# Performance work log

Hardware: AMD Instinct MI355X
Metric: run time of the kernel (lower is better)

Reference implementation:

```python
import jax, jax.numpy as jnp
import numpy as np

B = 2          # graphs (images)
GRID = 13      # patches per spatial dim -> N = 169 patches per image
N = GRID * GRID
NN = B * N     # total nodes
C = 256        # hidden_dim / out_channels per head
H = 4          # attention heads
L = 3          # GAT layers
LRELU_SLOPE = 0.2
LN_EPS = 1e-5


def _dense_edges():
    # fully-connected directed graph (i != j) per image, as in create_graph
    idx = np.arange(N)
    src, dst = np.meshgrid(idx, idx, indexing='ij')
    mask = src != dst
    src, dst = src[mask], dst[mask]              # [N*(N-1)]
    offs = (np.arange(B) * N)[:, None]
    e_src = (src[None, :] + offs).reshape(-1)
    e_dst = (dst[None, :] + offs).reshape(-1)
    return e_src.astype(np.int32), e_dst.astype(np.int32)


def setup_inputs() -> dict:
    key = jax.random.key(0)
    ks = jax.random.split(key, 8)
    s = 0.05
    e_src, e_dst = _dense_edges()
    return {
        'x':   jax.random.normal(ks[0], (NN, C), jnp.float32),
        'Wl':  jax.random.normal(ks[1], (L, C, H * C), jnp.float32) * s,
        'bl':  jnp.zeros((L, H * C), jnp.float32),
        'Wr':  jax.random.normal(ks[2], (L, C, H * C), jnp.float32) * s,
        'br':  jnp.zeros((L, H * C), jnp.float32),
        'att': jax.random.normal(ks[3], (L, H, C), jnp.float32) * s,
        'bias': jnp.zeros((L, C), jnp.float32),
        'ln_g': jnp.ones((L, C), jnp.float32),
        'ln_b': jnp.zeros((L, C), jnp.float32),
        'W1':  jax.random.normal(ks[4], (L, C, 2 * C), jnp.float32) * s,
        'b1':  jnp.zeros((L, 2 * C), jnp.float32),
        'W2':  jax.random.normal(ks[5], (L, 2 * C, C), jnp.float32) * s,
        'b2':  jnp.zeros((L, C), jnp.float32),
        'edge_src': jnp.asarray(e_src),
        'edge_dst': jnp.asarray(e_dst),
        'batch_ids': jnp.repeat(jnp.arange(B, dtype=jnp.int32), N),
    }


def _gatv2(x, Wl, bl, Wr, br, att, bias, src, dst, n_nodes):
    # PyG GATv2Conv, concat=False (mean over heads)
    xl = (x @ Wl + bl).reshape(n_nodes, H, C)   # source transform
    xr = (x @ Wr + br).reshape(n_nodes, H, C)   # target transform
    e = jax.nn.leaky_relu(xl[src] + xr[dst], LRELU_SLOPE)     # [E,H,C]
    logits = jnp.einsum('ehc,hc->eh', e, att)                 # [E,H]
    m = jax.ops.segment_max(logits, dst, num_segments=n_nodes)
    a = jnp.exp(logits - m[dst])
    z = jax.ops.segment_sum(a, dst, num_segments=n_nodes)
    alpha = a / (z[dst] + 1e-16)                              # softmax per target
    msg = alpha[:, :, None] * xl[src]                         # [E,H,C]
    agg = jax.ops.segment_sum(msg, dst, num_segments=n_nodes) # [N,H,C]
    return agg.mean(axis=1) + bias


def _layernorm(x, g, b):
    mu = x.mean(-1, keepdims=True)
    var = jnp.mean((x - mu) ** 2, -1, keepdims=True)
    return (x - mu) * jax.lax.rsqrt(var + LN_EPS) * g + b


def reference(x, Wl, bl, Wr, br, att, bias, ln_g, ln_b, W1, b1, W2, b2,
              edge_src, edge_dst, batch_ids):
    n_nodes = x.shape[0]
    for l in range(L):
        residual = x
        h = _gatv2(x, Wl[l], bl[l], Wr[l], br[l], att[l], bias[l],
                   edge_src, edge_dst, n_nodes)
        h = _layernorm(h, ln_g[l], ln_b[l])
        mlp = jnp.maximum(h @ W1[l] + b1[l], 0.0) @ W2[l] + b2[l]
        x = residual + mlp
    # global mean pool per graph
    sums = jax.ops.segment_sum(x, batch_ids, num_segments=B)
    cnts = jax.ops.segment_sum(jnp.ones((n_nodes, 1), x.dtype), batch_ids,
                               num_segments=B)
    return sums / cnts
```

## Files before the change

kernel.cpp:

```cpp
#include <hip/hip_runtime.h>
#include <hip/hip_bf16.h>

typedef __hip_bfloat16 bf16;
typedef __attribute__((ext_vector_type(8))) short short8v;
typedef __attribute__((ext_vector_type(4))) float float4v;

#define NNODES 169
#define NNTOT  338
#define CH     256
#define NH     4
#define NL     3
#define SPAD   176
#define LN_EPS 1e-5f

__device__ __forceinline__ float b2f(bf16 v) { return __bfloat162float(v); }
__device__ __forceinline__ float lrelu(float v) { return fmaxf(v, 0.2f * v); }
__device__ __forceinline__ float ldm(const void* p, size_t i, int isbf) {
    return isbf ? b2f(((const bf16*)p)[i]) : ((const float*)p)[i];
}
__device__ __forceinline__ short f2bf(float f) {
    union { float f; unsigned u; } x; x.f = f;
    return (short)((x.u + 0x7FFFu + ((x.u >> 16) & 1u)) >> 16);
}
__device__ __forceinline__ int sniff_bf(const void* lng) {
    return ((((const unsigned*)lng)[0] & 0xFFFFu) == 0x3F80u) ? 1 : 0;
}

__global__ __launch_bounds__(256) void k_wt(
    const void* __restrict__ Wl, const void* __restrict__ Wr,
    const void* __restrict__ W1, const void* __restrict__ W2,
    short* __restrict__ wlT, short* __restrict__ wrT,
    short* __restrict__ w1T, short* __restrict__ w2T,
    const void* __restrict__ lng)
{
    __shared__ float s_t[32][33];
    const int isbf = sniff_bf(lng);
    const int z = blockIdx.z, mat = z & 3, l = z >> 2;
    const void* src; short* dst; int K, N;
    if      (mat == 0) { src = Wl; dst = wlT; K = CH;     N = NH * CH; }
    else if (mat == 1) { src = Wr; dst = wrT; K = CH;     N = NH * CH; }
    else if (mat == 2) { src = W1; dst = w1T; K = CH;     N = 2 * CH;  }
    else               { src = W2; dst = w2T; K = 2 * CH; N = CH;      }
    const int tiles = (K >> 5) * (N >> 5);
    if ((int)blockIdx.x >= tiles) return;
    const int tn = blockIdx.x % (N >> 5), tk = blockIdx.x / (N >> 5);
    const int k0 = tk * 32, n0 = tn * 32;
    const size_t lKN = (size_t)l * K * N;
    const int tx = threadIdx.x & 31, ty = threadIdx.x >> 5;

    for (int r = ty; r < 32; r += 8)
        s_t[r][tx] = ldm(src, lKN + (size_t)(k0 + r) * N + n0 + tx, isbf);
    __syncthreads();
    for (int r = ty; r < 32; r += 8)
        dst[lKN + (size_t)(n0 + r) * K + k0 + tx] = f2bf(s_t[tx][r]);
}

template<int KK, int ACT, int RES, int XLT>
__device__ __forceinline__ void mfma_gemm(
    short* __restrict__ sA, short* __restrict__ sBT,
    const void* __restrict__ Av, int a_bf,
    const short* __restrict__ WT,
    const void* __restrict__ bv_, size_t oB, int isbf,
    const void* __restrict__ x_res, int r_bf,
    float* __restrict__ out, float* __restrict__ xlT,
    int M, int N, int row0, int col0)
{
    const int STR = KK + 8;
    const int tid = threadIdx.x, lane = tid & 63, w = tid >> 6;
    const int r = tid >> 2, q = tid & 3;
    const int kseg = KK / 4, kb0 = q * kseg;
    const int m = lane & 15, kb = (lane >> 4) * 8;
    const int w16 = w * 16;

    {
        const int gr = row0 + r;
        const int ok = (gr < M);
        if (a_bf) {
            const bf16* ap = (const bf16*)Av + (size_t)gr * KK + kb0;
            #pragma unroll
            for (int j = 0; j < kseg; j += 8) {
                int4 v = ok ? *(const int4*)(ap + j) : make_int4(0, 0, 0, 0);
                *(int4*)&sA[r * STR + kb0 + j] = v;
            }
        } else {
            const float* ap = (const float*)Av + (size_t)gr * KK + kb0;
            #pragma unroll
            for (int j = 0; j < kseg; j += 8) {
                short v8[8];
                if (ok) {
                    const float4 f0 = *(const float4*)(ap + j);
                    const float4 f1 = *(const float4*)(ap + j + 4);
                    v8[0] = f2bf(f0.x); v8[1] = f2bf(f0.y);
                    v8[2] = f2bf(f0.z); v8[3] = f2bf(f0.w);
                    v8[4] = f2bf(f1.x); v8[5] = f2bf(f1.y);
                    v8[6] = f2bf(f1.z); v8[7] = f2bf(f1.w);
                } else {
                    #pragma unroll
                    for (int u = 0; u < 8; u++) v8[u] = 0;
                }
                *(int4*)&sA[r * STR + kb0 + j] = *(int4*)v8;
            }
        }
        const short* bp = WT + (size_t)(col0 + r) * KK + kb0;
        #pragma unroll
        for (int j = 0; j < kseg; j += 8)
            *(int4*)&sBT[r * STR + kb0 + j] = *(const int4*)(bp + j);
    }
    __syncthreads();

    float4v acc[4];
    #pragma unroll
    for (int t = 0; t < 4; t++) acc[t] = (float4v){0.f, 0.f, 0.f, 0.f};

    #pragma unroll
    for (int kc = 0; kc < KK / 32; kc++) {
        const short8v af = *(const short8v*)&sA[(w16 + m) * STR + kc * 32 + kb];
        #pragma unroll
        for (int t = 0; t < 4; t++) {
            const short8v bfv = *(const short8v*)&sBT[(t * 16 + m) * STR + kc * 32 + kb];
            acc[t] = __builtin_amdgcn_mfma_f32_16x16x32_bf16(af, bfv, acc[t], 0, 0, 0);
        }
    }

    const int rq = (lane >> 4) * 4;
    #pragma unroll
    for (int t = 0; t < 4; t++) {
        const int col = col0 + t * 16 + m;
        const float bias_v = ldm(bv_, oB + col, isbf);
        #pragma unroll
        for (int rr = 0; rr < 4; rr++) {
            const int gr = row0 + w16 + rq + rr;
            if (gr >= M) continue;
            float v = acc[t][rr] + bias_v;
            if (ACT) v = fmaxf(v, 0.f);
            if (RES) v += ldm(x_res, (size_t)gr * N + col, r_bf);
            out[(size_t)gr * N + col] = v;
            if (XLT) {
                const int hh = col >> 8, cc = col & 255;
                const int gg = (gr >= NNODES) ? 1 : 0;
                const int ss = gr - gg * NNODES;
                xlT[((size_t)(gg * NH + hh) * CH + cc) * SPAD + ss] = v;
            }
        }
    }
}

__global__ __launch_bounds__(256) void k_gemm_lr(
    const void* __restrict__ Av, int israw,
    const short* __restrict__ wlT, const short* __restrict__ wrT, size_t oWT,
    const void* __restrict__ bl, const void* __restrict__ br, size_t oB,
    float* __restrict__ xl, float* __restrict__ xr, float* __restrict__ xlT,
    const void* __restrict__ lng)
{
    __shared__ short sA[64 * 264];
    __shared__ short sBT[64 * 264];
    const int isbf = sniff_bf(lng);
    const int a_bf = israw ? isbf : 0;
    const int row0 = blockIdx.x * 64, col0 = blockIdx.y * 64;
    if (blockIdx.z == 0)
        mfma_gemm<256,0,0,1>(sA, sBT, Av, a_bf, wlT + oWT, bl, oB, isbf,
                             nullptr, 0, xl, xlT, NNTOT, NH * CH, row0, col0);
    else
        mfma_gemm<256,0,0,0>(sA, sBT, Av, a_bf, wrT + oWT, br, oB, isbf,
                             nullptr, 0, xr, nullptr, NNTOT, NH * CH, row0, col0);
}

__global__ __launch_bounds__(256) void k_mlp1(
    const float* __restrict__ A, const short* __restrict__ w1T, size_t oWT,
    const void* __restrict__ b, size_t oB,
    float* __restrict__ out, const void* __restrict__ lng)
{
    __shared__ short sA[64 * 264];
    __shared__ short sBT[64 * 264];
    const int isbf = sniff_bf(lng);
    mfma_gemm<256,1,0,0>(sA, sBT, A, 0, w1T + oWT, b, oB, isbf, nullptr, 0,
                         out, nullptr, NNTOT, 2 * CH, blockIdx.x * 64, blockIdx.y * 64);
}

__global__ __launch_bounds__(256) void k_mlp2(
    const float* __restrict__ A, const short* __restrict__ w2T, size_t oWT,
    const void* __restrict__ b, size_t oB,
    const void* __restrict__ x_res, int israw,
    float* __restrict__ out, const void* __restrict__ lng)
{
    __shared__ short sA[64 * 520];
    __shared__ short sBT[64 * 520];
    const int isbf = sniff_bf(lng);
    const int r_bf = israw ? isbf : 0;
    mfma_gemm<512,0,1,0>(sA, sBT, A, 0, w2T + oWT, b, oB, isbf, x_res, r_bf,
                         out, nullptr, NNTOT, CH, blockIdx.x * 64, blockIdx.y * 64);
}

__global__ __launch_bounds__(256) void k_logits_sm(
    const float* __restrict__ xlT, const float* __restrict__ xr,
    const void* __restrict__ att, size_t oA,
    float* __restrict__ alphaR, const void* __restrict__ lng)
{
    __shared__ float s_att[CH];
    __shared__ float s_xr[4 * CH];
    __shared__ float s_tile[64 * SPAD];
    __shared__ float s_log[4 * SPAD];
    const int isbf = sniff_bf(lng);
    const int g = blockIdx.z, h = blockIdx.y, d0 = blockIdx.x * 4;
    const int tid = threadIdx.x, lane = tid & 63, wv = tid >> 6;

    s_att[tid] = ldm(att, oA + h * CH + tid, isbf);
    #pragma unroll
    for (int i = 0; i < 4; i++) {
        const int d = d0 + i;
        s_xr[i * CH + tid] = (d < NNODES)
            ? xr[(size_t)(g * NNODES + d) * (NH * CH) + h * CH + tid] : 0.f;
    }

    float l0 = 0.f, l1 = 0.f, l2 = 0.f, l3 = 0.f;
    const int s = tid;
    const float4* src = (const float4*)(xlT + ((size_t)(g * NH + h) * CH) * SPAD);
    for (int ch = 0; ch < 4; ch++) {
        __syncthreads();
        for (int i = tid; i < 64 * SPAD / 4; i += 256)
            ((float4*)s_tile)[i] = src[ch * (64 * SPAD / 4) + i];
        __syncthreads();
        if (s < NNODES) {
            const int cb = ch * 64;
            #pragma unroll 8
            for (int c = 0; c < 64; c++) {
                const float v = s_tile[c * SPAD + s];
                const float a = s_att[cb + c];
                l0 += a * lrelu(v + s_xr[cb + c]);
                l1 += a * lrelu(v + s_xr[CH + cb + c]);
                l2 += a * lrelu(v + s_xr[2 * CH + cb + c]);
                l3 += a * lrelu(v + s_xr[3 * CH + cb + c]);
            }
        }
    }
    if (s < NNODES) {
        s_log[s] = l0; s_log[SPAD + s] = l1;
        s_log[2 * SPAD + s] = l2; s_log[3 * SPAD + s] = l3;
    }
    __syncthreads();

    {
        const int d = d0 + wv;
        const float* row = s_log + wv * SPAD;
        const int s0 = lane, s1 = lane + 64, s2 = lane + 128;
        const float v0 = (s0 < NNODES && s0 != d) ? row[s0] : -1e30f;
        const float v1 = (s1 < NNODES && s1 != d) ? row[s1] : -1e30f;
        const float v2 = (s2 < NNODES && s2 != d) ? row[s2] : -1e30f;
        float mx = fmaxf(v0, fmaxf(v1, v2));
        mx = fmaxf(mx, __shfl_xor(mx, 32)); mx = fmaxf(mx, __shfl_xor(mx, 16));
        mx = fmaxf(mx, __shfl_xor(mx, 8));  mx = fmaxf(mx, __shfl_xor(mx, 4));
        mx = fmaxf(mx, __shfl_xor(mx, 2));  mx = fmaxf(mx, __shfl_xor(mx, 1));
        const float e0 = expf(v0 - mx), e1 = expf(v1 - mx), e2 = expf(v2 - mx);
        float z = e0 + e1 + e2;
        z += __shfl_xor(z, 32); z += __shfl_xor(z, 16); z += __shfl_xor(z, 8);
        z += __shfl_xor(z, 4);  z += __shfl_xor(z, 2);  z += __shfl_xor(z, 1);
        const float sc = 0.25f / (z + 1e-16f);
        if (d < NNODES) {
            float* arow = alphaR + ((size_t)(g * NH + h) * NNODES + d) * SPAD;
            if (s0 < NNODES) arow[s0] = e0 * sc;
            if (s1 < NNODES) arow[s1] = e1 * sc;
            if (s2 < NNODES) arow[s2] = e2 * sc;
        }
    }
}

__global__ __launch_bounds__(256) void k_agg(
    const float* __restrict__ alphaR, const float* __restrict__ xl,
    float* __restrict__ part)
{
    __shared__ float s_a[32 * 33];
    __shared__ float s_x[32 * 64];
    const int gh = blockIdx.z, g = gh >> 2, h = gh & 3;
    const int d0 = blockIdx.x * 32, c0 = blockIdx.y * 64;
    const int tid = threadIdx.x;
    const int dr = (tid >> 4) * 2, cq = (tid & 15) * 4;
    const int sr = tid >> 3, sc4 = (tid & 7) * 4;
    const int xc8 = (tid & 7) * 8;

    float acc[2][4] = {{0.f,0.f,0.f,0.f},{0.f,0.f,0.f,0.f}};

    for (int s0 = 0; s0 < NNODES; s0 += 32) {
        __syncthreads();
        {
            const int d = d0 + sr;
            const float* ap = alphaR + ((size_t)gh * NNODES + d) * SPAD + s0 + sc4;
            const int ok = (d < NNODES);
            s_a[sr * 33 + sc4 + 0] = (ok && s0 + sc4 + 0 < NNODES) ? ap[0] : 0.f;
            s_a[sr * 33 + sc4 + 1] = (ok && s0 + sc4 + 1 < NNODES) ? ap[1] : 0.f;
            s_a[sr * 33 + sc4 + 2] = (ok && s0 + sc4 + 2 < NNODES) ? ap[2] : 0.f;
            s_a[sr * 33 + sc4 + 3] = (ok && s0 + sc4 + 3 < NNODES) ? ap[3] : 0.f;
        }
        {
            const int sg = s0 + sr;
            if (sg < NNODES) {
                const float* xp = xl + (size_t)(g * NNODES + sg) * (NH * CH) + h * CH + c0 + xc8;
                *(float4*)&s_x[sr * 64 + xc8]     = *(const float4*)(xp);
                *(float4*)&s_x[sr * 64 + xc8 + 4] = *(const float4*)(xp + 4);
            } else {
                #pragma unroll
                for (int j = 0; j < 8; j++) s_x[sr * 64 + xc8 + j] = 0.f;
            }
        }
        __syncthreads();
        #pragma unroll
        for (int k = 0; k < 32; k++) {
            const float a0 = s_a[(dr + 0) * 33 + k];
            const float a1 = s_a[(dr + 1) * 33 + k];
            const float4 xv = *(const float4*)&s_x[k * 64 + cq];
            acc[0][0] += a0 * xv.x; acc[0][1] += a0 * xv.y;
            acc[0][2] += a0 * xv.z; acc[0][3] += a0 * xv.w;
            acc[1][0] += a1 * xv.x; acc[1][1] += a1 * xv.y;
            acc[1][2] += a1 * xv.z; acc[1][3] += a1 * xv.w;
        }
    }
    #pragma unroll
    for (int i = 0; i < 2; i++) {
        const int d = d0 + dr + i;
        if (d >= NNODES) continue;
        float4 v;
        v.x = acc[i][0]; v.y = acc[i][1]; v.z = acc[i][2]; v.w = acc[i][3];
        *(float4*)(part + ((size_t)h * NNTOT + g * NNODES + d) * CH + c0 + cq) = v;
    }
}

__global__ __launch_bounds__(256) void k_ln(
    const float* __restrict__ part,
    const void* __restrict__ bias, size_t oB,
    const void* __restrict__ ln_g, size_t oG,
    const void* __restrict__ ln_b, size_t oBt,
    float* __restrict__ h_out, const void* __restrict__ lng)
{
    __shared__ float s_red[8];
    const int isbf = sniff_bf(lng);
    const int node = blockIdx.x, c = threadIdx.x;
    const int lane = c & 63, wv = c >> 6;

    float vch = part[((size_t)0 * NNTOT + node) * CH + c]
              + part[((size_t)1 * NNTOT + node) * CH + c]
              + part[((size_t)2 * NNTOT + node) * CH + c]
              + part[((size_t)3 * NNTOT + node) * CH + c]
              + ldm(bias, oB + c, isbf);

    float s1 = vch, s2 = vch * vch;
    s1 += __shfl_xor(s1, 32); s2 += __shfl_xor(s2, 32);
    s1 += __shfl_xor(s1, 16); s2 += __shfl_xor(s2, 16);
    s1 += __shfl_xor(s1, 8);  s2 += __shfl_xor(s2, 8);
    s1 += __shfl_xor(s1, 4);  s2 += __shfl_xor(s2, 4);
    s1 += __shfl_xor(s1, 2);  s2 += __shfl_xor(s2, 2);
    s1 += __shfl_xor(s1, 1);  s2 += __shfl_xor(s2, 1);
    if (lane == 0) { s_red[wv] = s1; s_red[4 + wv] = s2; }
    __syncthreads();
    const float S1 = s_red[0] + s_red[1] + s_red[2] + s_red[3];
    const float S2 = s_red[4] + s_red[5] + s_red[6] + s_red[7];
    const float mu  = S1 * (1.f / CH);
    const float var = S2 * (1.f / CH) - mu * mu;
    const float o = (vch - mu) * rsqrtf(var + LN_EPS) * ldm(ln_g, oG + c, isbf)
                  + ldm(ln_b, oBt + c, isbf);
    h_out[(size_t)node * CH + c] = o;
}

__global__ __launch_bounds__(256) void k_pool(const float* __restrict__ x,
                                              void* __restrict__ out,
                                              const void* __restrict__ lng) {
    const int isbf = sniff_bf(lng);
    const int g = blockIdx.x, c = threadIdx.x;
    float s = 0.f;
    const float* p = x + (size_t)g * NNODES * CH + c;
    #pragma unroll 8
    for (int n = 0; n < NNODES; n++) s += p[(size_t)n * CH];
    const float v = s * (1.f / NNODES);
    if (isbf) ((bf16*)out)[g * CH + c] = __float2bfloat16(v);
    else      ((float*)out)[g * CH + c] = v;
}

extern "C" void kernel_launch(void* const* d_in, const int* in_sizes, int n_in,
                              void* d_out, int out_size, void* d_ws, size_t ws_size,
                              hipStream_t stream)
{
    const void* x_in = d_in[0];
    const void* Wl   = d_in[1];
    const void* bl   = d_in[2];
    const void* Wr   = d_in[3];
    const void* br   = d_in[4];
    const void* att  = d_in[5];
    const void* bias = d_in[6];
    const void* lng  = d_in[7];
    const void* lnb  = d_in[8];
    const void* W1   = d_in[9];
    const void* b1   = d_in[10];
    const void* W2   = d_in[11];
    const void* b2   = d_in[12];

    float* ws     = (float*)d_ws;
    float* xl     = ws;
    float* xr     = xl + (size_t)NNTOT * NH * CH;
    float* xlT    = xr + (size_t)NNTOT * NH * CH;
    float* alphaR = xlT + (size_t)2 * NH * CH * SPAD;
    float* part   = alphaR + (size_t)2 * NH * NNODES * SPAD;
    float* h_ln   = part + (size_t)NH * NNTOT * CH;
    float* m1     = h_ln + (size_t)NNTOT * CH;
    float* xa     = m1 + (size_t)NNTOT * 2 * CH;
    float* xb     = xa + (size_t)NNTOT * CH;
    short* wlT    = (short*)(xb + (size_t)NNTOT * CH);
    short* wrT    = wlT + (size_t)NL * CH * NH * CH;
    short* w1T    = wrT + (size_t)NL * CH * NH * CH;
    short* w2T    = w1T + (size_t)NL * CH * 2 * CH;

    const size_t sB  = NH * CH;
    const size_t sA  = NH * CH;
    const size_t sC  = CH;
    const size_t sB1 = 2 * CH;
    const size_t sWT  = (size_t)CH * NH * CH;
    const size_t sW1T = (size_t)CH * 2 * CH;
    const size_t sW2T = (size_t)2 * CH * CH;

    k_wt<<<dim3(256, 1, 12), 256, 0, stream>>>(
        Wl, Wr, W1, W2, wlT, wrT, w1T, w2T, lng);

    const void* x_l[3] = { x_in, xa, xb };
    float*      x_o[3] = { xa, xb, xa };

    for (int l = 0; l < NL; l++) {
        const int israw = (l == 0);
        k_gemm_lr<<<dim3(6, 16, 2), 256, 0, stream>>>(
            x_l[l], israw, wlT, wrT, (size_t)l * sWT,
            bl, br, (size_t)l * sB, xl, xr, xlT, lng);
        k_logits_sm<<<dim3(43, NH, 2), 256, 0, stream>>>(
            xlT, xr, att, (size_t)l * sA, alphaR, lng);
        k_agg<<<dim3(6, 4, 8), 256, 0, stream>>>(alphaR, xl, part);
        k_ln<<<dim3(NNTOT), 256, 0, stream>>>(
            part, bias, (size_t)l * sC, lng, (size_t)l * sC, lnb, (size_t)l * sC,
            h_ln, lng);
        k_mlp1<<<dim3(6, 8), 256, 0, stream>>>(
            h_ln, w1T, (size_t)l * sW1T, b1, (size_t)l * sB1, m1, lng);
        k_mlp2<<<dim3(6, 4), 256, 0, stream>>>(
            m1, w2T, (size_t)l * sW2T, b2, (size_t)l * sC,
            x_l[l], israw, x_o[l], lng);
    }

    k_pool<<<dim3(2), 256, 0, stream>>>(xa, d_out, lng);
}
```

Before: 321.8 us.

## Fuse MLP GEMMs into one kernel and drop transposed xl buffer

Merges the two MLP GEMM kernels into one k_mlp kernel. Each block holds 16 rows, keeps the ReLU hidden activations in shared memory as bf16, and streams W1 and W2 tiles through LDS, so the m1 round trip through global memory and one launch per layer go away. It also stops writing the transposed xlT copy in the xl GEMM epilogue. The logits kernel instead reads xl row-major and transposes it into a padded shared tile. The cost is fewer blocks for the MLP (22), each streaming all of W1 and W2, which lowers parallelism and multiplies weight traffic.

```diff
diff --git a/kernel.cpp b/kernel.cpp
--- a/kernel.cpp
+++ b/kernel.cpp
@@ -11,6 +11,8 @@
 #define NH     4
 #define NL     3
 #define SPAD   176
+#define TPAD   177
+#define M1PAD  536
 #define LN_EPS 1e-5f
 
 __device__ __forceinline__ float b2f(bf16 v) { return __bfloat162float(v); }
@@ -55,14 +57,14 @@
         dst[lKN + (size_t)(n0 + r) * K + k0 + tx] = f2bf(s_t[tx][r]);
 }
 
-template<int KK, int ACT, int RES, int XLT>
+template<int KK, int ACT, int RES>
 __device__ __forceinline__ void mfma_gemm(
     short* __restrict__ sA, short* __restrict__ sBT,
     const void* __restrict__ Av, int a_bf,
     const short* __restrict__ WT,
     const void* __restrict__ bv_, size_t oB, int isbf,
     const void* __restrict__ x_res, int r_bf,
-    float* __restrict__ out, float* __restrict__ xlT,
+    float* __restrict__ out,
     int M, int N, int row0, int col0)
 {
     const int STR = KK + 8;
@@ -135,12 +137,6 @@
             if (ACT) v = fmaxf(v, 0.f);
             if (RES) v += ldm(x_res, (size_t)gr * N + col, r_bf);
             out[(size_t)gr * N + col] = v;
-            if (XLT) {
-                const int hh = col >> 8, cc = col & 255;
-                const int gg = (gr >= NNODES) ? 1 : 0;
-                const int ss = gr - gg * NNODES;
-                xlT[((size_t)(gg * NH + hh) * CH + cc) * SPAD + ss] = v;
-            }
         }
     }
 }
@@ -149,7 +145,7 @@
     const void* __restrict__ Av, int israw,
     const short* __restrict__ wlT, const short* __restrict__ wrT, size_t oWT,
     const void* __restrict__ bl, const void* __restrict__ br, size_t oB,
-    float* __restrict__ xl, float* __restrict__ xr, float* __restrict__ xlT,
+    float* __restrict__ xl, float* __restrict__ xr,
     const void* __restrict__ lng)
 {
     __shared__ short sA[64 * 264];
@@ -158,47 +154,21 @@
     const int a_bf = israw ? isbf : 0;
     const int row0 = blockIdx.x * 64, col0 = blockIdx.y * 64;
     if (blockIdx.z == 0)
-        mfma_gemm<256,0,0,1>(sA, sBT, Av, a_bf, wlT + oWT, bl, oB, isbf,
-                             nullptr, 0, xl, xlT, NNTOT, NH * CH, row0, col0);
+        mfma_gemm<256,0,0>(sA, sBT, Av, a_bf, wlT + oWT, bl, oB, isbf,
+                           nullptr, 0, xl, NNTOT, NH * CH, row0, col0);
     else
-        mfma_gemm<256,0,0,0>(sA, sBT, Av, a_bf, wrT + oWT, br, oB, isbf,
-                             nullptr, 0, xr, nullptr, NNTOT, NH * CH, row0, col0);
-}
-
-__global__ __launch_bounds__(256) void k_mlp1(
-    const float* __restrict__ A, const short* __restrict__ w1T, size_t oWT,
-    const void* __restrict__ b, size_t oB,
-    float* __restrict__ out, const void* __restrict__ lng)
-{
-    __shared__ short sA[64 * 264];
-    __shared__ short sBT[64 * 264];
-    const int isbf = sniff_bf(lng);
-    mfma_gemm<256,1,0,0>(sA, sBT, A, 0, w1T + oWT, b, oB, isbf, nullptr, 0,
-                         out, nullptr, NNTOT, 2 * CH, blockIdx.x * 64, blockIdx.y * 64);
-}
-
-__global__ __launch_bounds__(256) void k_mlp2(
-    const float* __restrict__ A, const short* __restrict__ w2T, size_t oWT,
-    const void* __restrict__ b, size_t oB,
-    const void* __restrict__ x_res, int israw,
-    float* __restrict__ out, const void* __restrict__ lng)
-{
-    __shared__ short sA[64 * 520];
-    __shared__ short sBT[64 * 520];
-    const int isbf = sniff_bf(lng);
-    const int r_bf = israw ? isbf : 0;
-    mfma_gemm<512,0,1,0>(sA, sBT, A, 0, w2T + oWT, b, oB, isbf, x_res, r_bf,
-                         out, nullptr, NNTOT, CH, blockIdx.x * 64, blockIdx.y * 64);
+        mfma_gemm<256,0,0>(sA, sBT, Av, a_bf, wrT + oWT, br, oB, isbf,
+                           nullptr, 0, xr, NNTOT, NH * CH, row0, col0);
 }
 
 __global__ __launch_bounds__(256) void k_logits_sm(
-    const float* __restrict__ xlT, const float* __restrict__ xr,
+    const float* __restrict__ xl, const float* __restrict__ xr,
     const void* __restrict__ att, size_t oA,
     float* __restrict__ alphaR, const void* __restrict__ lng)
 {
     __shared__ float s_att[CH];
     __shared__ float s_xr[4 * CH];
-    __shared__ float s_tile[64 * SPAD];
+    __shared__ float s_tile[64 * TPAD];
     __shared__ float s_log[4 * SPAD];
     const int isbf = sniff_bf(lng);
     const int g = blockIdx.z, h = blockIdx.y, d0 = blockIdx.x * 4;
@@ -214,17 +184,25 @@
 
     float l0 = 0.f, l1 = 0.f, l2 = 0.f, l3 = 0.f;
     const int s = tid;
-    const float4* src = (const float4*)(xlT + ((size_t)(g * NH + h) * CH) * SPAD);
     for (int ch = 0; ch < 4; ch++) {
         __syncthreads();
-        for (int i = tid; i < 64 * SPAD / 4; i += 256)
-            ((float4*)s_tile)[i] = src[ch * (64 * SPAD / 4) + i];
+        for (int i = tid; i < SPAD * 16; i += 256) {
+            const int si = i >> 4, c4 = (i & 15) * 4;
+            const float4 v = (si < NNODES)
+                ? *(const float4*)(xl + (size_t)(g * NNODES + si) * (NH * CH)
+                                   + h * CH + ch * 64 + c4)
+                : make_float4(0.f, 0.f, 0.f, 0.f);
+            s_tile[(c4 + 0) * TPAD + si] = v.x;
+            s_tile[(c4 + 1) * TPAD + si] = v.y;
+            s_tile[(c4 + 2) * TPAD + si] = v.z;
+            s_tile[(c4 + 3) * TPAD + si] = v.w;
+        }
         __syncthreads();
         if (s < NNODES) {
             const int cb = ch * 64;
             #pragma unroll 8
             for (int c = 0; c < 64; c++) {
-                const float v = s_tile[c * SPAD + s];
+                const float v = s_tile[c * TPAD + s];
                 const float a = s_att[cb + c];
                 l0 += a * lrelu(v + s_xr[cb + c]);
                 l1 += a * lrelu(v + s_xr[CH + cb + c]);
@@ -359,6 +337,86 @@
     h_out[(size_t)node * CH + c] = o;
 }
 
+__global__ __launch_bounds__(256) void k_mlp(
+    const float* __restrict__ h_ln,
+    const short* __restrict__ w1T, size_t oW1T,
+    const void* __restrict__ b1, size_t oB1,
+    const short* __restrict__ w2T, size_t oW2T,
+    const void* __restrict__ b2, size_t oB2,
+    const void* __restrict__ x_res, int israw,
+    float* __restrict__ out, const void* __restrict__ lng)
+{
+    __shared__ short sA[16 * 264];
+    __shared__ short sM1[16 * M1PAD];
+    __shared__ short sW[64 * 520];
+    const int isbf = sniff_bf(lng);
+    const int r_bf = israw ? isbf : 0;
+    const int g = blockIdx.y;
+    const int d0 = blockIdx.x * 16;
+    const int tid = threadIdx.x, lane = tid & 63, w = tid >> 6;
+    const int m = lane & 15, kb = (lane >> 4) * 8, rq = (lane >> 4) * 4;
+    const int w16 = w * 16;
+
+    for (int i = tid; i < 16 * 64; i += 256) {
+        const int si = i >> 6, c4 = (i & 63) * 4;
+        const int d = d0 + si;
+        const float4 v = (d < NNODES)
+            ? *(const float4*)(h_ln + (size_t)(g * NNODES + d) * CH + c4)
+            : make_float4(0.f, 0.f, 0.f, 0.f);
+        short v4[4] = { f2bf(v.x), f2bf(v.y), f2bf(v.z), f2bf(v.w) };
+        *(int2*)&sA[si * 264 + c4] = *(int2*)v4;
+    }
+
+    for (int nc = 0; nc < 8; nc++) {
+        __syncthreads();
+        for (int i = tid; i < 64 * 32; i += 256) {
+            const int r = i >> 5, k8 = (i & 31) * 8;
+            *(int4*)&sW[r * 264 + k8] =
+                *(const int4*)(w1T + oW1T + (size_t)(nc * 64 + r) * 256 + k8);
+        }
+        __syncthreads();
+        float4v acc = {0.f, 0.f, 0.f, 0.f};
+        #pragma unroll
+        for (int kc = 0; kc < 8; kc++) {
+            const short8v af = *(const short8v*)&sA[m * 264 + kc * 32 + kb];
+            const short8v bfv = *(const short8v*)&sW[(w16 + m) * 264 + kc * 32 + kb];
+            acc = __builtin_amdgcn_mfma_f32_16x16x32_bf16(af, bfv, acc, 0, 0, 0);
+        }
+        const int ng = nc * 64 + w16 + m;
+        const float bv = ldm(b1, oB1 + ng, isbf);
+        #pragma unroll
+        for (int rr = 0; rr < 4; rr++)
+            sM1[(rq + rr) * M1PAD + ng] = f2bf(fmaxf(acc[rr] + bv, 0.f));
+    }
+
+    for (int nc = 0; nc < 4; nc++) {
+        __syncthreads();
+        for (int i = tid; i < 64 * 64; i += 256) {
+            const int r = i >> 6, k8 = (i & 63) * 8;
+            *(int4*)&sW[r * 520 + k8] =
+                *(const int4*)(w2T + oW2T + (size_t)(nc * 64 + r) * 512 + k8);
+        }
+        __syncthreads();
+        float4v acc = {0.f, 0.f, 0.f, 0.f};
+        #pragma unroll
+        for (int kc = 0; kc < 16; kc++) {
+            const short8v af = *(const short8v*)&sM1[m * M1PAD + kc * 32 + kb];
+            const short8v bfv = *(const short8v*)&sW[(w16 + m) * 520 + kc * 32 + kb];
+            acc = __builtin_amdgcn_mfma_f32_16x16x32_bf16(af, bfv, acc, 0, 0, 0);
+        }
+        const int ng = nc * 64 + w16 + m;
+        const float bv = ldm(b2, oB2 + ng, isbf);
+        #pragma unroll
+        for (int rr = 0; rr < 4; rr++) {
+            const int d = d0 + rq + rr;
+            if (d < NNODES) {
+                const size_t ro = (size_t)(g * NNODES + d) * CH + ng;
+                out[ro] = acc[rr] + bv + ldm(x_res, ro, r_bf);
+            }
+        }
+    }
+}
+
 __global__ __launch_bounds__(256) void k_pool(const float* __restrict__ x,
                                               void* __restrict__ out,
                                               const void* __restrict__ lng) {
@@ -394,12 +452,10 @@
     float* ws     = (float*)d_ws;
     float* xl     = ws;
     float* xr     = xl + (size_t)NNTOT * NH * CH;
-    float* xlT    = xr + (size_t)NNTOT * NH * CH;
-    float* alphaR = xlT + (size_t)2 * NH * CH * SPAD;
+    float* alphaR = xr + (size_t)NNTOT * NH * CH;
     float* part   = alphaR + (size_t)2 * NH * NNODES * SPAD;
     float* h_ln   = part + (size_t)NH * NNTOT * CH;
-    float* m1     = h_ln + (size_t)NNTOT * CH;
-    float* xa     = m1 + (size_t)NNTOT * 2 * CH;
+    float* xa     = h_ln + (size_t)NNTOT * CH;
     float* xb     = xa + (size_t)NNTOT * CH;
     short* wlT    = (short*)(xb + (size_t)NNTOT * CH);
     short* wrT    = wlT + (size_t)NL * CH * NH * CH;
@@ -424,17 +480,16 @@
         const int israw = (l == 0);
         k_gemm_lr<<<dim3(6, 16, 2), 256, 0, stream>>>(
             x_l[l], israw, wlT, wrT, (size_t)l * sWT,
-            bl, br, (size_t)l * sB, xl, xr, xlT, lng);
+            bl, br, (size_t)l * sB, xl, xr, lng);
         k_logits_sm<<<dim3(43, NH, 2), 256, 0, stream>>>(
-            xlT, xr, att, (size_t)l * sA, alphaR, lng);
+            xl, xr, att, (size_t)l * sA, alphaR, lng);
         k_agg<<<dim3(6, 4, 8), 256, 0, stream>>>(alphaR, xl, part);
         k_ln<<<dim3(NNTOT), 256, 0, stream>>>(
             part, bias, (size_t)l * sC, lng, (size_t)l * sC, lnb, (size_t)l * sC,
             h_ln, lng);
-        k_mlp1<<<dim3(6, 8), 256, 0, stream>>>(
-            h_ln, w1T, (size_t)l * sW1T, b1, (size_t)l * sB1, m1, lng);
-        k_mlp2<<<dim3(6, 4), 256, 0, stream>>>(
-            m1, w2T, (size_t)l * sW2T, b2, (size_t)l * sC,
+        k_mlp<<<dim3(11, 2), 256, 0, stream>>>(
+            h_ln, w1T, (size_t)l * sW1T, b1, (size_t)l * sB1,
+            w2T, (size_t)l * sW2T, b2, (size_t)l * sC,
             x_l[l], israw, x_o[l], lng);
     }
 
```

Result: slower. 395.2 us (+22.8%).
